# Kernel optimization log

Hardware: AMD Instinct MI355X
Metric: run time of the kernel (lower is better)

Reference implementation:

```python
import jax, jax.numpy as jnp
import numpy as np

# Additive (Bahdanau) attention from Attention_1.
# Original torch code materializes h = f1[:,None,:,:] + f2[:,:,None,:] (N,T,L,D)
# then applies fc: Linear(D,1). Since fc is linear, the score separates:
#   score[n,t,l] = f1[n,l]@w + f2[n,t]@w + b
# which is mathematically identical and avoids the O(N*T*L*D) intermediate.

D = 1024

def setup_inputs() -> dict:
    key = jax.random.key(0)
    k1, k2, k3, k4 = jax.random.split(key, 4)
    feature_1 = jax.random.normal(k1, (64, 512, D), dtype=jnp.float32)  # N,L,D
    feature_2 = jax.random.normal(k2, (64, 128, D), dtype=jnp.float32)  # N,T,D
    # fc params: torch Linear(D,1) -> weight (1,D), bias (1); use vector + scalar
    bound = 1.0 / np.sqrt(D)
    w = jax.random.uniform(k3, (D,), minval=-bound, maxval=bound, dtype=jnp.float32)
    b = jax.random.uniform(k4, (), minval=-bound, maxval=bound, dtype=jnp.float32)
    return {"feature_1": feature_1, "feature_2": feature_2, "w": w, "b": b}

def reference(feature_1, feature_2, w, b):
    # scores: [N,T,L] = (f2@w)[:,:,None] + (f1@w)[:,None,:] + b
    s1 = jnp.einsum("nld,d->nl", feature_1, w)  # [N,L]
    s2 = jnp.einsum("ntd,d->nt", feature_2, w)  # [N,T]
    att = jax.nn.softmax(s2[:, :, None] + s1[:, None, :] + b, axis=2)  # [N,T,L]
    f_hat = jnp.einsum("ntl,nld->ntd", att, feature_1)  # [N,T,D]
    return (f_hat, att)
```

## Files before the change

### kernel.cpp

```cpp
#include <hip/hip_runtime.h>
#include <math.h>


#define N 64
#define L 512
#define T 128
#define D 1024
#define CPN 16
#define RPW 8

typedef float f4 __attribute__((ext_vector_type(4)));

__global__ __launch_bounds__(256) void k1_fused(const float* __restrict__ f1,
                                                const float* __restrict__ w,
                                                float* __restrict__ e,
                                                float* __restrict__ zpart,
                                                float* __restrict__ gpart) {
    __shared__ f4 lds4[4][4][64];
    __shared__ float zred[4];
    int blk  = blockIdx.x;
    int n    = blk >> 4;
    int c    = blk & 15;
    int wid  = threadIdx.x >> 6;
    int lane = threadIdx.x & 63;
    int l0   = c * 32 + wid * RPW;

    const f4* w4 = (const f4*)w;
    f4 wf[4];
#pragma unroll
    for (int k = 0; k < 4; ++k) wf[k] = w4[k * 64 + lane];

    f4 acc[4] = {{0,0,0,0},{0,0,0,0},{0,0,0,0},{0,0,0,0}};
    float zsum = 0.f;
    float ekeep = 0.f;
    const f4* base = (const f4*)(f1 + ((size_t)(n * L + l0)) * D);

#pragma unroll
    for (int j = 0; j < RPW; j += 2) {
        f4 va[4], vb[4];
#pragma unroll
        for (int k = 0; k < 4; ++k)
            va[k] = __builtin_nontemporal_load(&base[(size_t)j * (D / 4) + k * 64 + lane]);
#pragma unroll
        for (int k = 0; k < 4; ++k)
            vb[k] = __builtin_nontemporal_load(&base[(size_t)(j + 1) * (D / 4) + k * 64 + lane]);

        float da = 0.f, db = 0.f;
#pragma unroll
        for (int k = 0; k < 4; ++k) {
            da += va[k].x * wf[k].x + va[k].y * wf[k].y + va[k].z * wf[k].z + va[k].w * wf[k].w;
            db += vb[k].x * wf[k].x + vb[k].y * wf[k].y + vb[k].z * wf[k].z + vb[k].w * wf[k].w;
        }
#pragma unroll
        for (int off = 32; off; off >>= 1) {
            da += __shfl_xor(da, off, 64);
            db += __shfl_xor(db, off, 64);
        }
        float ea = __expf(da);
        float eb = __expf(db);
        zsum += ea + eb;
        if (lane == j)     ekeep = ea;
        if (lane == j + 1) ekeep = eb;
#pragma unroll
        for (int k = 0; k < 4; ++k) {
            acc[k].x += ea * va[k].x + eb * vb[k].x;
            acc[k].y += ea * va[k].y + eb * vb[k].y;
            acc[k].z += ea * va[k].z + eb * vb[k].z;
            acc[k].w += ea * va[k].w + eb * vb[k].w;
        }
    }

#pragma unroll
    for (int k = 0; k < 4; ++k) lds4[wid][k][lane] = acc[k];
    if (lane == 0) zred[wid] = zsum;
    if (lane < RPW) e[n * L + l0 + lane] = ekeep;
    __syncthreads();

    int k = wid;
    f4 s = lds4[0][k][lane];
#pragma unroll
    for (int ww = 1; ww < 4; ++ww) {
        f4 v = lds4[ww][k][lane];
        s.x += v.x; s.y += v.y; s.z += v.z; s.w += v.w;
    }
    ((f4*)gpart)[(size_t)blk * (D / 4) + k * 64 + lane] = s;
    if (threadIdx.x == 0) zpart[blk] = zred[0] + zred[1] + zred[2] + zred[3];
}

__global__ __launch_bounds__(256) void k2_out(const float* __restrict__ gpart,
                                              const float* __restrict__ zpart,
                                              const float* __restrict__ e,
                                              float* __restrict__ out) {
    const int FH4 = N * T * (D / 4);
    int b = blockIdx.x;
    int t = threadIdx.x;
    if (b < 1024) {
        int n  = b >> 4;
        int tt = (b & 15) * 8;
        float z = 0.f;
#pragma unroll
        for (int c = 0; c < CPN; ++c) z += zpart[n * CPN + c];
        float inv = 1.f / z;
        const f4* gp = (const f4*)gpart + ((size_t)n * CPN) * (D / 4) + t;
        f4 s = {0.f, 0.f, 0.f, 0.f};
#pragma unroll
        for (int c = 0; c < CPN; ++c) {
            f4 v = gp[(size_t)c * (D / 4)];
            s.x += v.x; s.y += v.y; s.z += v.z; s.w += v.w;
        }
        s.x *= inv; s.y *= inv; s.z *= inv; s.w *= inv;
        f4* o = (f4*)out + (size_t)n * (T * D / 4) + (size_t)tt * (D / 4) + t;
#pragma unroll
        for (int j = 0; j < 8; ++j)
            __builtin_nontemporal_store(s, &o[(size_t)j * (D / 4)]);
    } else {
        int idx = b - 1024;
        int n  = idx >> 3;
        int tt = (idx & 7) * 16;
        int l4   = t & 127;
        int half = t >> 7;
        float z = 0.f;
#pragma unroll
        for (int c = 0; c < CPN; ++c) z += zpart[n * CPN + c];
        float inv = 1.f / z;
        f4 pv = ((const f4*)e)[n * (L / 4) + l4];
        pv.x *= inv; pv.y *= inv; pv.z *= inv; pv.w *= inv;
        f4* o = (f4*)out + FH4 + (size_t)n * (T * L / 4);
#pragma unroll
        for (int j = 0; j < 8; ++j) {
            int row = tt + j * 2 + half;
            __builtin_nontemporal_store(pv, &o[(size_t)row * (L / 4) + l4]);
        }
    }
}

extern "C" void kernel_launch(void* const* d_in, const int* in_sizes, int n_in,
                              void* d_out, int out_size, void* d_ws, size_t ws_size,
                              hipStream_t stream) {
    const float* f1 = (const float*)d_in[0];
    const float* w  = (const float*)d_in[2];
    float* out = (float*)d_out;

    float* ws    = (float*)d_ws;
    float* e     = ws;
    float* zpart = e + N * L;
    float* gpart = zpart + N * CPN;

    k1_fused<<<N * CPN, 256, 0, stream>>>(f1, w, e, zpart, gpart);
    k2_out  <<<1536, 256, 0, stream>>>(gpart, zpart, e, out);
}
```

Baseline: 221.8 us.

## Fuse both phases into one cooperative kernel with grid sync

Merges the partial-reduction kernel and the output-broadcast kernel into a single cooperative launch that uses a grid-wide barrier between phases, with the old two-kernel path kept as a fallback if the cooperative launch fails. This removes one kernel launch and the gap between launches. In exchange it adds grid-sync cost, and the output-writing phase now runs on 1024 blocks instead of 1536. Running all blocks co-resident requires up to 4 blocks per CU via launch bounds.

```diff
diff --git a/kernel.cpp b/kernel.cpp
--- a/kernel.cpp
+++ b/kernel.cpp
@@ -1,5 +1,8 @@
 #include <hip/hip_runtime.h>
+#include <hip/hip_cooperative_groups.h>
 #include <math.h>
+
+namespace cg = cooperative_groups;
 
 
 #define N 64
@@ -11,11 +14,11 @@
 
 typedef float f4 __attribute__((ext_vector_type(4)));
 
-__global__ __launch_bounds__(256) void k1_fused(const float* __restrict__ f1,
-                                                const float* __restrict__ w,
-                                                float* __restrict__ e,
-                                                float* __restrict__ zpart,
-                                                float* __restrict__ gpart) {
+__device__ __forceinline__ void do_phase1(const float* __restrict__ f1,
+                                          const float* __restrict__ w,
+                                          float* __restrict__ e,
+                                          float* __restrict__ zpart,
+                                          float* __restrict__ gpart) {
     __shared__ f4 lds4[4][4][64];
     __shared__ float zred[4];
     int blk  = blockIdx.x;
@@ -85,6 +88,61 @@
     }
     ((f4*)gpart)[(size_t)blk * (D / 4) + k * 64 + lane] = s;
     if (threadIdx.x == 0) zpart[blk] = zred[0] + zred[1] + zred[2] + zred[3];
+}
+
+__global__ __launch_bounds__(256, 4) void k_fused_all(const float* __restrict__ f1,
+                                                      const float* __restrict__ w,
+                                                      float* __restrict__ e,
+                                                      float* __restrict__ zpart,
+                                                      float* __restrict__ gpart,
+                                                      float* __restrict__ out) {
+    do_phase1(f1, w, e, zpart, gpart);
+
+    __threadfence();
+    cg::this_grid().sync();
+    __threadfence();
+
+    const int FH4 = N * T * (D / 4);
+    int b = blockIdx.x;
+    int t = threadIdx.x;
+    int n = b >> 4;
+    int q = b & 15;
+    float z = 0.f;
+#pragma unroll
+    for (int c = 0; c < CPN; ++c) z += zpart[n * CPN + c];
+    float inv = 1.f / z;
+
+    const f4* gp = (const f4*)gpart + ((size_t)n * CPN) * (D / 4) + t;
+    f4 s = {0.f, 0.f, 0.f, 0.f};
+#pragma unroll
+    for (int c = 0; c < CPN; ++c) {
+        f4 v = gp[(size_t)c * (D / 4)];
+        s.x += v.x; s.y += v.y; s.z += v.z; s.w += v.w;
+    }
+    s.x *= inv; s.y *= inv; s.z *= inv; s.w *= inv;
+    f4* o = (f4*)out + (size_t)n * (T * D / 4) + (size_t)(q * 8) * (D / 4) + t;
+#pragma unroll
+    for (int j = 0; j < 8; ++j)
+        __builtin_nontemporal_store(s, &o[(size_t)j * (D / 4)]);
+
+    int l4   = t & 127;
+    int half = t >> 7;
+    f4 pv = ((const f4*)e)[n * (L / 4) + l4];
+    pv.x *= inv; pv.y *= inv; pv.z *= inv; pv.w *= inv;
+    f4* oa = (f4*)out + FH4 + (size_t)n * (T * L / 4);
+#pragma unroll
+    for (int j = 0; j < 4; ++j) {
+        int row = q * 8 + j * 2 + half;
+        __builtin_nontemporal_store(pv, &oa[(size_t)row * (L / 4) + l4]);
+    }
+}
+
+__global__ __launch_bounds__(256) void k1_fused(const float* __restrict__ f1,
+                                                const float* __restrict__ w,
+                                                float* __restrict__ e,
+                                                float* __restrict__ zpart,
+                                                float* __restrict__ gpart) {
+    do_phase1(f1, w, e, zpart, gpart);
 }
 
 __global__ __launch_bounds__(256) void k2_out(const float* __restrict__ gpart,
@@ -146,6 +204,13 @@
     float* zpart = e + N * L;
     float* gpart = zpart + N * CPN;
 
-    k1_fused<<<N * CPN, 256, 0, stream>>>(f1, w, e, zpart, gpart);
-    k2_out  <<<1536, 256, 0, stream>>>(gpart, zpart, e, out);
-}
+    void* args[] = {(void*)&f1, (void*)&w, (void*)&e,
+                    (void*)&zpart, (void*)&gpart, (void*)&out};
+    hipError_t st = hipLaunchCooperativeKernel((const void*)k_fused_all,
+                                               dim3(N * CPN), dim3(256),
+                                               args, 0, stream);
+    if (st != hipSuccess) {
+        k1_fused<<<N * CPN, 256, 0, stream>>>(f1, w, e, zpart, gpart);
+        k2_out  <<<1536, 256, 0, stream>>>(gpart, zpart, e, out);
+    }
+}
```

Result: slower. 525.2 us (+136.8%).
